# Performance work log

Measured on AMD Instinct MI355X. Metric: run time of the kernel, lower is better.

Reference implementation:

```python
import jax, jax.numpy as jnp
from jax import lax
import numpy as np

GAMMA, WARP = 0.01, 134.4          # SoftDTW(gamma=0.01, warp=134.4)
INF, BIG = 100000.0, 1e9           # INF from kl_loss_sdtw; BIG ~ math.inf boundary
KL_A, KL_FWD_A, GEN_A, GEN_E2E_A, FEAT_A, DUR_A, MEL_A = 1.0, 1.0, 1.0, 1.0, 1.0, 1.0, 45.0


def soft_dtw(D):
    """Soft-DTW with warp penalty. D: [B, N, M] -> R[:, N, M].
    R[i,j] = D[i-1,j-1] + softmin_gamma(R[i-1,j-1], R[i-1,j]+warp, R[i,j-1]+warp)."""
    B, N, M = D.shape
    row0 = jnp.full((B, M + 1), BIG, D.dtype).at[:, 0].set(0.0)  # R[0, :]

    def row_step(prev_row, d_row):                 # prev_row: [B, M+1], d_row: [B, M]
        left0 = jnp.full((B,), BIG, D.dtype)       # R[i, 0]

        def col_step(r_left, inp):
            d, r_diag, r_up = inp                  # each [B]
            r0 = -r_diag / GAMMA
            r1 = -(r_up + WARP) / GAMMA
            r2 = -(r_left + WARP) / GAMMA
            rmax = jnp.maximum(jnp.maximum(r0, r1), r2)
            smin = -GAMMA * (jnp.log(jnp.exp(r0 - rmax) + jnp.exp(r1 - rmax) + jnp.exp(r2 - rmax)) + rmax)
            r = d + smin
            return r, r

        xs = (d_row.T, prev_row[:, :-1].T, prev_row[:, 1:].T)   # scan over j=1..M
        _, vals = lax.scan(col_step, left0, xs)                 # [M, B]
        new_row = jnp.concatenate([left0[:, None], vals.T], axis=1)
        return new_row, None

    last, _ = lax.scan(row_step, row0, jnp.swapaxes(D, 0, 1))   # scan over i=1..N
    return last[:, M]


def sdtw_kl_matrix(z, logs_q, m, logs_p):
    """kl[b,i,j] = sum_h logs_p - logs_q - 0.5 + 0.5*(z-m)^2*exp(-2 logs_p).
    m, logs_p: [b,h,tp]; z, logs_q: [b,h,tq] -> [b,tp,tq] via 3 batched GEMMs."""
    h = m.shape[1]
    w = jnp.exp(-2.0 * logs_p)                                   # [b,h,tp]
    quad = (jnp.einsum('bhi,bhj->bij', w, z * z)
            - 2.0 * jnp.einsum('bhi,bhj->bij', w * m, z)
            + jnp.sum(w * m * m, axis=1)[:, :, None])
    return (jnp.sum(logs_p, axis=1)[:, :, None]
            - jnp.sum(logs_q, axis=1)[:, None, :]
            - 0.5 * h + 0.5 * quad)


def kl_loss_sdtw(z, logs_q, m, logs_p, p_mask, q_mask):
    kl = sdtw_kl_matrix(z, logs_q, m, logs_p)
    kl = jnp.pad(kl, ((0, 0), (0, 1), (0, 1)))
    pm = jnp.pad(p_mask, ((0, 0), (0, 1)))
    qm = jnp.pad(q_mask, ((0, 0), (0, 1)))
    pb = pm[:, :, None].astype(bool)
    qb = qm[:, None, :].astype(bool)
    kl = jnp.where(pb ^ qb, INF, kl)
    kl = jnp.where((~pb) & (~qb), 0.0, kl)
    return jnp.sum(soft_dtw(kl)) / jnp.sum(pm)


def _forward(mel_slice, mel_slice_hat, scores_disc_fake, scores_disc_fake_e2e,
             feats_disc_real, feats_disc_fake, loss_duration, loss_duration_len,
             loss_pitch, z_p, m_p, logs_p, z_q, m_q, logs_q, p_mask, z_mask):
    # generator losses: sum over discriminators of mean((1-score)^2)
    loss_gen = jnp.sum(jnp.mean((1.0 - scores_disc_fake) ** 2, axis=(1, 2))) * GEN_A
    loss_gen_e2e = jnp.sum(jnp.mean((1.0 - scores_disc_fake_e2e) ** 2, axis=(1, 2))) * GEN_E2E_A
    # feature-matching loss (real feats detached)
    fr = lax.stop_gradient(feats_disc_real)
    loss_fm = jnp.sum(jnp.mean(jnp.abs(fr - feats_disc_fake), axis=(1, 2, 3))) * 2.0 * FEAT_A
    loss_mel = jnp.mean(jnp.abs(mel_slice - mel_slice_hat)) * MEL_A
    loss_dur = jnp.sum(loss_duration) * DUR_A
    loss_dur_len = jnp.log(loss_duration_len + 1e-6)
    zm = z_mask[:, 0, :]
    loss_kl = kl_loss_sdtw(z_p, logs_q, m_p, logs_p, p_mask, zm) * KL_A
    loss_kl_fwd = kl_loss_sdtw(z_q, logs_p, m_q, logs_q, zm, p_mask) * KL_FWD_A
    return (loss_gen + loss_gen_e2e + loss_fm + loss_mel + loss_dur
            + loss_dur_len + loss_kl + loss_kl_fwd)


def setup_inputs() -> dict:
    key = jax.random.key(0)
    ks = jax.random.split(key, 16)
    B, H, TP, TQ = 4, 192, 350, 400
    return {
        'mel_slice': jax.random.normal(ks[0], (B, 80, 128), jnp.float32),
        'mel_slice_hat': jax.random.normal(ks[1], (B, 80, 128), jnp.float32),
        'scores_disc_fake': jax.random.normal(ks[2], (6, B, 8192), jnp.float32),
        'scores_disc_fake_e2e': jax.random.normal(ks[3], (6, B, 8192), jnp.float32),
        'feats_disc_real': jax.random.normal(ks[4], (24, B, 128, 4096), jnp.float32),
        'feats_disc_fake': jax.random.normal(ks[5], (24, B, 128, 4096), jnp.float32),
        'loss_duration': jax.random.uniform(ks[6], (B, TP), jnp.float32) * 0.01,
        'loss_duration_len': jax.random.uniform(ks[7], (), jnp.float32) + 0.5,
        'loss_pitch': jax.random.uniform(ks[8], (B, TP), jnp.float32),
        'z_p': jax.random.normal(ks[9], (B, H, TQ), jnp.float32),
        'm_p': jax.random.normal(ks[10], (B, H, TP), jnp.float32),
        'logs_p': 0.1 * jax.random.normal(ks[11], (B, H, TP), jnp.float32),
        'z_q': jax.random.normal(ks[12], (B, H, TP), jnp.float32),
        'm_q': jax.random.normal(ks[13], (B, H, TQ), jnp.float32),
        'logs_q': 0.1 * jax.random.normal(ks[14], (B, H, TQ), jnp.float32),
        'p_mask': jnp.ones((B, TP), jnp.float32),
        'z_mask': jnp.ones((B, 1, TQ), jnp.float32),
    }


def reference(mel_slice, mel_slice_hat, scores_disc_fake, scores_disc_fake_e2e,
              feats_disc_real, feats_disc_fake, loss_duration, loss_duration_len,
              loss_pitch, z_p, m_p, logs_p, z_q, m_q, logs_q, p_mask, z_mask):
    return _forward(mel_slice, mel_slice_hat, scores_disc_fake, scores_disc_fake_e2e,
                    feats_disc_real, feats_disc_fake, loss_duration, loss_duration_len,
                    loss_pitch, z_p, m_p, logs_p, z_q, m_q, logs_q, p_mask, z_mask)
```

## Files before the change

kernel.cpp:

```cpp
#include <hip/hip_runtime.h>
#include <math.h>

#define GAMMA_ 0.01f
#define WARP_  134.4f
#define INFV   100000.0f
#define BIGV   1000000000.0f

#define B_  4
#define H_  192
#define TP_ 350
#define TQ_ 400

#define ACC_OFF 0
#define DTW_OFF 16
#define SLP_OFF 32
#define SLQ_OFF (SLP_OFF + B_*TP_)
#define KL1_OFF 3072
#define KL1_NCOL 401
#define KL1_PITCHT 352
#define KL2_OFF (KL1_OFF + B_*KL1_NCOL*KL1_PITCHT)
#define KL2_NCOL 351
#define KL2_PITCHT 408

#define RING_SLOTS 67
#define RING_PITCH 416

typedef float f4_t __attribute__((ext_vector_type(4)));

__device__ __forceinline__ unsigned pk2(float a, float b) {
    unsigned ua = __float_as_uint(a), ub = __float_as_uint(b);
    ua = (ua + 0x7FFFu + ((ua >> 16) & 1u)) >> 16;
    ub = (ub + 0x7FFFu + ((ub >> 16) & 1u)) & 0xFFFF0000u;
    return ua | ub;
}
__device__ __forceinline__ int modS(int x) { return x - (x / RING_SLOTS) * RING_SLOTS; }

__global__ void sl_kernel(const float* __restrict__ logs_p,
                          const float* __restrict__ logs_q,
                          const float* __restrict__ pmask,
                          const float* __restrict__ zmask,
                          float* __restrict__ ws) {
    if (blockIdx.x == 12) {
        int tid = threadIdx.x;
        float a5 = 0.f, a6 = 0.f;
        for (int v = tid; v < B_ * TP_; v += 256) a5 += pmask[v];
        for (int v = tid; v < B_ * TQ_; v += 256) a6 += zmask[v];
        __shared__ float s5[4], s6[4];
        for (int off = 32; off > 0; off >>= 1) { a5 += __shfl_xor(a5, off); a6 += __shfl_xor(a6, off); }
        if ((tid & 63) == 0) { s5[tid >> 6] = a5; s6[tid >> 6] = a6; }
        __syncthreads();
        if (tid == 0) {
            ws[5] = s5[0] + s5[1] + s5[2] + s5[3];
            ws[6] = s6[0] + s6[1] + s6[2] + s6[3];
        }
        return;
    }
    int t = blockIdx.x * 256 + threadIdx.x;
    if (t < 32 && t != 5 && t != 6) ws[ACC_OFF + t] = 0.f;
    if (t < B_ * TP_) {
        int b = t / TP_, i = t % TP_;
        const float* p = logs_p + (size_t)b * H_ * TP_ + i;
        float s = 0.f;
        for (int h = 0; h < H_; ++h) s += p[(size_t)h * TP_];
        ws[SLP_OFF + t] = s;
    } else if (t < B_ * TP_ + B_ * TQ_) {
        int t2 = t - B_ * TP_;
        int b = t2 / TQ_, j = t2 % TQ_;
        const float* p = logs_q + (size_t)b * H_ * TQ_ + j;
        float s = 0.f;
        for (int h = 0; h < H_; ++h) s += p[(size_t)h * TQ_];
        ws[SLQ_OFF + t2] = s;
    }
}

__global__ void kl_kernel(const float* __restrict__ mp, const float* __restrict__ lsp,
                          const float* __restrict__ zp,
                          const float* __restrict__ mq, const float* __restrict__ lsq,
                          const float* __restrict__ zq,
                          const float* __restrict__ pmask, const float* __restrict__ zmask,
                          float* __restrict__ ws) {
    int which = blockIdx.z >> 2;
    int b     = blockIdx.z & 3;
    const float *mS, *lS, *zS, *SLrow, *SLcol, *rm, *cm; float* out; int R, C, pitchT;
    if (which == 0) { mS=mp; lS=lsp; zS=zp; SLrow=ws+SLP_OFF; SLcol=ws+SLQ_OFF;
                      rm=pmask + b*TP_; cm=zmask + b*TQ_;
                      out=ws+KL1_OFF + (size_t)b*KL1_NCOL*KL1_PITCHT;
                      R=TP_; C=TQ_; pitchT=KL1_PITCHT; }
    else            { mS=mq; lS=lsq; zS=zq; SLrow=ws+SLQ_OFF; SLcol=ws+SLP_OFF;
                      rm=zmask + b*TQ_; cm=pmask + b*TP_;
                      out=ws+KL2_OFF + (size_t)b*KL2_NCOL*KL2_PITCHT;
                      R=TQ_; C=TP_; pitchT=KL2_PITCHT; }
    int i0 = blockIdx.x * 32;
    int j0 = blockIdx.y * 32;
    if (i0 > R || j0 > C) return;
    __shared__ __align__(16) float wS [16][32];
    __shared__ __align__(16) float mSh[16][32];
    __shared__ __align__(16) float zSh[16][32];
    const float* mB = mS + (size_t)b * H_ * R;
    const float* lB = lS + (size_t)b * H_ * R;
    const float* zB = zS + (size_t)b * H_ * C;
    int tx = threadIdx.x, ty = threadIdx.y;
    int t  = ty * 16 + tx;
    float a00 = 0.f, a01 = 0.f, a10 = 0.f, a11 = 0.f;
    for (int h0 = 0; h0 < H_; h0 += 16) {
        for (int e = t; e < 512; e += 256) {
            int hh = e >> 5, cc = e & 31;
            int h = h0 + hh;
            int gi = i0 + cc, gj = j0 + cc;
            float wv = 0.f, mv = 0.f;
            if (gi < R) {
                wv = __expf(-2.f * lB[(size_t)h * R + gi]);
                mv = mB[(size_t)h * R + gi];
            }
            wS[hh][cc] = wv; mSh[hh][cc] = mv;
            zSh[hh][cc] = (gj < C) ? zB[(size_t)h * C + gj] : 0.f;
        }
        __syncthreads();
#pragma unroll
        for (int kk = 0; kk < 16; ++kk) {
            float2 wv = *(const float2*)&wS [kk][tx * 2];
            float2 mv = *(const float2*)&mSh[kk][tx * 2];
            float2 zv = *(const float2*)&zSh[kk][ty * 2];
            float d;
            d = zv.x - mv.x; a00 += wv.x * d * d;
            d = zv.x - mv.y; a01 += wv.y * d * d;
            d = zv.y - mv.x; a10 += wv.x * d * d;
            d = zv.y - mv.y; a11 += wv.y * d * d;
        }
        __syncthreads();
    }
    float accs[2][2] = {{a00, a01}, {a10, a11}};
    for (int jj = 0; jj < 2; ++jj)
        for (int ii = 0; ii < 2; ++ii) {
            int I = i0 + tx * 2 + ii, J = j0 + ty * 2 + jj;
            if (I <= R && J <= C) {
                bool pbI = (I < R) && (rm[I] != 0.f);
                bool qbJ = (J < C) && (cm[J] != 0.f);
                float v;
                if (pbI & qbJ)
                    v = SLrow[b * R + I] - SLcol[b * C + J] - 0.5f * H_ + 0.5f * accs[jj][ii];
                else
                    v = (pbI ^ qbJ) ? INFV : 0.f;
                out[(size_t)J * pitchT + I] = v;
            }
        }
}

#define SLD(q, r, cc, ii, vv) { int col_ = ((q) << 3) + (cc); \
    if ((vv) && col_ <= C_) r = *(const f4_t*)(klT + (size_t)col_ * pitchT + ((ii) << 2)); }
#define SST(q, r, cc, ii, vv) { int col_ = ((q) << 3) + (cc); \
    if ((vv) && col_ <= C_) { int s_ = modS(col_); \
        uint2 u_; u_.x = pk2(r.x, r.y); u_.y = pk2(r.z, r.w); \
        *(uint2*)&ring[s_][(ii) << 2] = u_; } }

__global__ __launch_bounds__(512, 1) void dtw_kernel(float* ws) {
    __shared__ __align__(16) unsigned short ring[RING_SLOTS + 2][RING_PITCH];
    int bid = blockIdx.x, tid = threadIdx.x;
    int b = bid & 3, which = bid >> 2;
    int R_, C_, pitchT;
    const float* klT;
    if (which == 0) {
        R_ = TP_; C_ = TQ_; pitchT = KL1_PITCHT;
        klT = ws + KL1_OFF + (size_t)b * KL1_NCOL * KL1_PITCHT;
    } else {
        R_ = TQ_; C_ = TP_; pitchT = KL2_PITCHT;
        klT = ws + KL2_OFF + (size_t)b * KL2_NCOL * KL2_PITCHT;
    }
    int lres = R_ >> 3;
    int kres = R_ & 7;
    int tmax = C_ + lres;
    int P = (tmax >> 3) + 1;

    if (tid < 64) {
        int lane = tid; bool lane0 = (lane == 0);
        float p0=BIGV,p1=BIGV,p2=BIGV,p3=BIGV,p4=BIGV,p5=BIGV,p6=BIGV,p7=BIGV;
        float recv_cur = BIGV, recv_prev = BIGV;
        __syncthreads();
        for (int ph = 0; ph < P; ++ph) {
            int t0 = ph << 3;
            int c0 = t0 - lane;
            int cr = c0 < 0 ? 0 : (c0 > C_ ? C_ : c0);
            int s0 = modS(cr);
            int4 rd = *(const int4*)&ring[s0][lane << 3];
#pragma unroll
            for (int i = 0; i < 8; ++i) {
                int c = t0 + i - lane;
                int4 ru = rd;
                if (i < 7) {
                    int cn = c + 1; cn = cn < 0 ? 0 : (cn > C_ ? C_ : cn);
                    int sn = modS(cn);
                    rd = *(const int4*)&ring[sn][lane << 3];
                }
                float last_ = 0.f;
                if ((unsigned)c <= (unsigned)C_) {
                    float u_  = lane0 ? BIGV : recv_cur;
                    float dg  = (c == 0) ? (lane0 ? 0.f : BIGV) : (lane0 ? BIGV : recv_prev);
                    float d0 = __uint_as_float((unsigned)ru.x << 16);
                    float d1 = __uint_as_float((unsigned)ru.x & 0xFFFF0000u);
                    float d2 = __uint_as_float((unsigned)ru.y << 16);
                    float d3 = __uint_as_float((unsigned)ru.y & 0xFFFF0000u);
                    float d4 = __uint_as_float((unsigned)ru.z << 16);
                    float d5 = __uint_as_float((unsigned)ru.z & 0xFFFF0000u);
                    float d6 = __uint_as_float((unsigned)ru.w << 16);
                    float d7 = __uint_as_float((unsigned)ru.w & 0xFFFF0000u);
                    float B0 = WARP_ + d0, B1 = WARP_ + d1, B2 = WARP_ + d2, B3 = WARP_ + d3;
                    float B4 = WARP_ + d4, B5 = WARP_ + d5, B6 = WARP_ + d6, B7 = WARP_ + d7;
                    float P0 = fminf(dg + d0, p0 + B0);
                    float P1 = fminf(p0 + d1, p1 + B1);
                    float P2 = fminf(p1 + d2, p2 + B2);
                    float P3 = fminf(p2 + d3, p3 + B3);
                    float P4 = fminf(p3 + d4, p4 + B4);
                    float P5 = fminf(p4 + d5, p5 + B5);
                    float P6 = fminf(p5 + d6, p6 + B6);
                    float P7 = fminf(p6 + d7, p7 + B7);
                    u_ = fminf(P0, u_ + B0); p0 = u_;
                    u_ = fminf(P1, u_ + B1); p1 = u_;
                    u_ = fminf(P2, u_ + B2); p2 = u_;
                    u_ = fminf(P3, u_ + B3); p3 = u_;
                    u_ = fminf(P4, u_ + B4); p4 = u_;
                    u_ = fminf(P5, u_ + B5); p5 = u_;
                    u_ = fminf(P6, u_ + B6); p6 = u_;
                    u_ = fminf(P7, u_ + B7); p7 = u_;
                    last_ = u_;
                }
                recv_prev = recv_cur;
                recv_cur  = __shfl_up(last_, 1);
            }
            __syncthreads();
        }
        float q0 = __shfl(p0, lres), q1 = __shfl(p1, lres), q2 = __shfl(p2, lres),
              q3 = __shfl(p3, lres), q4 = __shfl(p4, lres), q5 = __shfl(p5, lres),
              q6 = __shfl(p6, lres), q7 = __shfl(p7, lres);
        if (lane0) {
            float res = (kres == 0) ? q0 : (kres == 1) ? q1 : (kres == 2) ? q2 :
                        (kres == 3) ? q3 : (kres == 4) ? q4 : (kres == 5) ? q5 :
                        (kres == 6) ? q6 : q7;
            ws[DTW_OFF + which * 4 + b] = res;
        }
    } else {
        int st  = tid - 64;
        int n4  = pitchT >> 2;
        int tot = n4 << 3;
        int cA = st / n4,  iA = st - cA * n4;
        int eB = st + 448; int cB = eB / n4, iB = eB - cB * n4;
        bool vA = st < tot, vB = eB < tot;
        f4_t rA = {0.f,0.f,0.f,0.f}, rB = {0.f,0.f,0.f,0.f};
        SLD(0, rA, cA, iA, vA) SLD(0, rB, cB, iB, vB)
        SST(0, rA, cA, iA, vA) SST(0, rB, cB, iB, vB)
        SLD(1, rA, cA, iA, vA) SLD(1, rB, cB, iB, vB)
        __syncthreads();
        for (int p = 0; p < P; ++p) {
            SST(p + 1, rA, cA, iA, vA) SST(p + 1, rB, cB, iB, vB)
            SLD(p + 2, rA, cA, iA, vA) SLD(p + 2, rB, cB, iB, vB)
            __syncthreads();
        }
    }
}

__global__ __launch_bounds__(512) void red_kernel(
    const float* __restrict__ mel, const float* __restrict__ melh,
    const float* __restrict__ sg,  const float* __restrict__ se,
    const float* __restrict__ fr,  const float* __restrict__ ff,
    const float* __restrict__ dur, float* ws) {
    __shared__ float sb[64];
    int tid = threadIdx.x;
    long T = (long)gridDim.x * 512;
    long gid = (long)blockIdx.x * 512 + tid;
    const float4* fr4   = (const float4*)fr;
    const float4* ff4   = (const float4*)ff;
    const float4* sg4   = (const float4*)sg;
    const float4* se4   = (const float4*)se;
    const float4* mel4  = (const float4*)mel;
    const float4* melh4 = (const float4*)melh;
    const float4* dur4  = (const float4*)dur;
    const long E0 = 12582912;
    float a2 = 0.f;
    long v = gid;
    for (; v + T < E0; v += 2 * T) {
        float4 x0 = fr4[v],     y0 = ff4[v];
        float4 x1 = fr4[v + T], y1 = ff4[v + T];
        a2 += fabsf(x0.x-y0.x)+fabsf(x0.y-y0.y)+fabsf(x0.z-y0.z)+fabsf(x0.w-y0.w);
        a2 += fabsf(x1.x-y1.x)+fabsf(x1.y-y1.y)+fabsf(x1.z-y1.z)+fabsf(x1.w-y1.w);
    }
    for (; v < E0; v += T) {
        float4 x = fr4[v], y = ff4[v];
        a2 += fabsf(x.x-y.x)+fabsf(x.y-y.y)+fabsf(x.z-y.z)+fabsf(x.w-y.w);
    }
    float a0=0.f, a1=0.f, a3=0.f, a4=0.f;
    long w = gid;
    if (w < 108894) {
        if (w < 49152) {
            float4 s = sg4[w]; float e;
            e=1.f-s.x; a0+=e*e; e=1.f-s.y; a0+=e*e; e=1.f-s.z; a0+=e*e; e=1.f-s.w; a0+=e*e;
        } else if (w < 98304) {
            float4 s = se4[w - 49152]; float e;
            e=1.f-s.x; a1+=e*e; e=1.f-s.y; a1+=e*e; e=1.f-s.z; a1+=e*e; e=1.f-s.w; a1+=e*e;
        } else if (w < 108544) {
            float4 x = mel4[w - 98304], y = melh4[w - 98304];
            a3 += fabsf(x.x-y.x)+fabsf(x.y-y.y)+fabsf(x.z-y.z)+fabsf(x.w-y.w);
        } else {
            float4 x = dur4[w - 108544]; a4 += x.x + x.y + x.z + x.w;
        }
    }
    float vals[5] = {a0, a1, a2, a3, a4};
#pragma unroll
    for (int q = 0; q < 5; ++q) {
        float x = vals[q];
        for (int off = 32; off > 0; off >>= 1) x += __shfl_xor(x, off);
        if ((tid & 63) == 0) sb[(tid >> 6) * 8 + q] = x;
    }
    __syncthreads();
    if (tid < 5) {
        float s = 0.f;
        for (int w2 = 0; w2 < 8; ++w2) s += sb[w2 * 8 + tid];
        atomicAdd(&ws[ACC_OFF + tid], s);
    }
}

__global__ void final_kernel(const float* __restrict__ ws,
                             const float* __restrict__ ldl,
                             float* __restrict__ out) {
    if (threadIdx.x == 0 && blockIdx.x == 0) {
        float gen  = ws[0] * (1.f / 32768.f);
        float e2e  = ws[1] * (1.f / 32768.f);
        float fm   = ws[2] * (2.f / 2097152.f);
        float melv = ws[3] * (45.f / 40960.f);
        float durv = ws[4];
        float dlen = logf(ldl[0] + 1e-6f);
        float kl  = (ws[DTW_OFF + 0] + ws[DTW_OFF + 1] + ws[DTW_OFF + 2] + ws[DTW_OFF + 3]) / ws[5];
        float klf = (ws[DTW_OFF + 4] + ws[DTW_OFF + 5] + ws[DTW_OFF + 6] + ws[DTW_OFF + 7]) / ws[6];
        out[0] = gen + e2e + fm + melv + durv + dlen + kl + klf;
    }
}

extern "C" void kernel_launch(void* const* d_in, const int* in_sizes, int n_in,
                              void* d_out, int out_size, void* d_ws, size_t ws_size,
                              hipStream_t stream) {
    const float* mel    = (const float*)d_in[0];
    const float* melh   = (const float*)d_in[1];
    const float* sg     = (const float*)d_in[2];
    const float* se     = (const float*)d_in[3];
    const float* fr     = (const float*)d_in[4];
    const float* ff     = (const float*)d_in[5];
    const float* dur    = (const float*)d_in[6];
    const float* ldl    = (const float*)d_in[7];
    const float* z_p    = (const float*)d_in[9];
    const float* m_p    = (const float*)d_in[10];
    const float* logs_p = (const float*)d_in[11];
    const float* z_q    = (const float*)d_in[12];
    const float* m_q    = (const float*)d_in[13];
    const float* logs_q = (const float*)d_in[14];
    const float* pmask  = (const float*)d_in[15];
    const float* zmask  = (const float*)d_in[16];
    float* ws  = (float*)d_ws;
    float* out = (float*)d_out;

    sl_kernel<<<13, 256, 0, stream>>>(logs_p, logs_q, pmask, zmask, ws);
    kl_kernel<<<dim3(13, 13, 8), dim3(16, 16), 0, stream>>>(
        m_p, logs_p, z_p, m_q, logs_q, z_q, pmask, zmask, ws);
    dtw_kernel<<<8, 512, 0, stream>>>(ws);
    red_kernel<<<1016, 512, 0, stream>>>(mel, melh, sg, se, fr, ff, dur, ws);
    final_kernel<<<1, 64, 0, stream>>>(ws, ldl, out);
}
```

Baseline: 206.6 us.

## Fuse DTW and reduction kernels so serial DTW overlaps bandwidth-bound reduction

Merges the 8-block DTW kernel and the large L1/MSE reduction kernel into one launch. The first 8 blocks run the serial DTW recurrence while the remaining 1016 blocks stream the feature tensors, so the latency-bound DTW hides behind the memory-bound reduction instead of running before it. The reduction also moves to nontemporal loads with a 4-way unroll. Risks: launch_bounds(512,1) now applies to the reduction blocks and may limit their occupancy, and the DTW blocks may share CUs with reduction blocks.

```diff
diff --git a/kernel.cpp b/kernel.cpp
--- a/kernel.cpp
+++ b/kernel.cpp
@@ -153,167 +153,176 @@
         uint2 u_; u_.x = pk2(r.x, r.y); u_.y = pk2(r.z, r.w); \
         *(uint2*)&ring[s_][(ii) << 2] = u_; } }
 
-__global__ __launch_bounds__(512, 1) void dtw_kernel(float* ws) {
-    __shared__ __align__(16) unsigned short ring[RING_SLOTS + 2][RING_PITCH];
-    int bid = blockIdx.x, tid = threadIdx.x;
-    int b = bid & 3, which = bid >> 2;
-    int R_, C_, pitchT;
-    const float* klT;
-    if (which == 0) {
-        R_ = TP_; C_ = TQ_; pitchT = KL1_PITCHT;
-        klT = ws + KL1_OFF + (size_t)b * KL1_NCOL * KL1_PITCHT;
-    } else {
-        R_ = TQ_; C_ = TP_; pitchT = KL2_PITCHT;
-        klT = ws + KL2_OFF + (size_t)b * KL2_NCOL * KL2_PITCHT;
-    }
-    int lres = R_ >> 3;
-    int kres = R_ & 7;
-    int tmax = C_ + lres;
-    int P = (tmax >> 3) + 1;
-
-    if (tid < 64) {
-        int lane = tid; bool lane0 = (lane == 0);
-        float p0=BIGV,p1=BIGV,p2=BIGV,p3=BIGV,p4=BIGV,p5=BIGV,p6=BIGV,p7=BIGV;
-        float recv_cur = BIGV, recv_prev = BIGV;
-        __syncthreads();
-        for (int ph = 0; ph < P; ++ph) {
-            int t0 = ph << 3;
-            int c0 = t0 - lane;
-            int cr = c0 < 0 ? 0 : (c0 > C_ ? C_ : c0);
-            int s0 = modS(cr);
-            int4 rd = *(const int4*)&ring[s0][lane << 3];
-#pragma unroll
-            for (int i = 0; i < 8; ++i) {
-                int c = t0 + i - lane;
-                int4 ru = rd;
-                if (i < 7) {
-                    int cn = c + 1; cn = cn < 0 ? 0 : (cn > C_ ? C_ : cn);
-                    int sn = modS(cn);
-                    rd = *(const int4*)&ring[sn][lane << 3];
-                }
-                float last_ = 0.f;
-                if ((unsigned)c <= (unsigned)C_) {
-                    float u_  = lane0 ? BIGV : recv_cur;
-                    float dg  = (c == 0) ? (lane0 ? 0.f : BIGV) : (lane0 ? BIGV : recv_prev);
-                    float d0 = __uint_as_float((unsigned)ru.x << 16);
-                    float d1 = __uint_as_float((unsigned)ru.x & 0xFFFF0000u);
-                    float d2 = __uint_as_float((unsigned)ru.y << 16);
-                    float d3 = __uint_as_float((unsigned)ru.y & 0xFFFF0000u);
-                    float d4 = __uint_as_float((unsigned)ru.z << 16);
-                    float d5 = __uint_as_float((unsigned)ru.z & 0xFFFF0000u);
-                    float d6 = __uint_as_float((unsigned)ru.w << 16);
-                    float d7 = __uint_as_float((unsigned)ru.w & 0xFFFF0000u);
-                    float B0 = WARP_ + d0, B1 = WARP_ + d1, B2 = WARP_ + d2, B3 = WARP_ + d3;
-                    float B4 = WARP_ + d4, B5 = WARP_ + d5, B6 = WARP_ + d6, B7 = WARP_ + d7;
-                    float P0 = fminf(dg + d0, p0 + B0);
-                    float P1 = fminf(p0 + d1, p1 + B1);
-                    float P2 = fminf(p1 + d2, p2 + B2);
-                    float P3 = fminf(p2 + d3, p3 + B3);
-                    float P4 = fminf(p3 + d4, p4 + B4);
-                    float P5 = fminf(p4 + d5, p5 + B5);
-                    float P6 = fminf(p5 + d6, p6 + B6);
-                    float P7 = fminf(p6 + d7, p7 + B7);
-                    u_ = fminf(P0, u_ + B0); p0 = u_;
-                    u_ = fminf(P1, u_ + B1); p1 = u_;
-                    u_ = fminf(P2, u_ + B2); p2 = u_;
-                    u_ = fminf(P3, u_ + B3); p3 = u_;
-                    u_ = fminf(P4, u_ + B4); p4 = u_;
-                    u_ = fminf(P5, u_ + B5); p5 = u_;
-                    u_ = fminf(P6, u_ + B6); p6 = u_;
-                    u_ = fminf(P7, u_ + B7); p7 = u_;
-                    last_ = u_;
-                }
-                recv_prev = recv_cur;
-                recv_cur  = __shfl_up(last_, 1);
-            }
-            __syncthreads();
-        }
-        float q0 = __shfl(p0, lres), q1 = __shfl(p1, lres), q2 = __shfl(p2, lres),
-              q3 = __shfl(p3, lres), q4 = __shfl(p4, lres), q5 = __shfl(p5, lres),
-              q6 = __shfl(p6, lres), q7 = __shfl(p7, lres);
-        if (lane0) {
-            float res = (kres == 0) ? q0 : (kres == 1) ? q1 : (kres == 2) ? q2 :
-                        (kres == 3) ? q3 : (kres == 4) ? q4 : (kres == 5) ? q5 :
-                        (kres == 6) ? q6 : q7;
-            ws[DTW_OFF + which * 4 + b] = res;
-        }
-    } else {
-        int st  = tid - 64;
-        int n4  = pitchT >> 2;
-        int tot = n4 << 3;
-        int cA = st / n4,  iA = st - cA * n4;
-        int eB = st + 448; int cB = eB / n4, iB = eB - cB * n4;
-        bool vA = st < tot, vB = eB < tot;
-        f4_t rA = {0.f,0.f,0.f,0.f}, rB = {0.f,0.f,0.f,0.f};
-        SLD(0, rA, cA, iA, vA) SLD(0, rB, cB, iB, vB)
-        SST(0, rA, cA, iA, vA) SST(0, rB, cB, iB, vB)
-        SLD(1, rA, cA, iA, vA) SLD(1, rB, cB, iB, vB)
-        __syncthreads();
-        for (int p = 0; p < P; ++p) {
-            SST(p + 1, rA, cA, iA, vA) SST(p + 1, rB, cB, iB, vB)
-            SLD(p + 2, rA, cA, iA, vA) SLD(p + 2, rB, cB, iB, vB)
-            __syncthreads();
-        }
-    }
-}
-
-__global__ __launch_bounds__(512) void red_kernel(
+__global__ __launch_bounds__(512, 1) void main_kernel(
     const float* __restrict__ mel, const float* __restrict__ melh,
     const float* __restrict__ sg,  const float* __restrict__ se,
     const float* __restrict__ fr,  const float* __restrict__ ff,
     const float* __restrict__ dur, float* ws) {
-    __shared__ float sb[64];
-    int tid = threadIdx.x;
-    long T = (long)gridDim.x * 512;
-    long gid = (long)blockIdx.x * 512 + tid;
-    const float4* fr4   = (const float4*)fr;
-    const float4* ff4   = (const float4*)ff;
-    const float4* sg4   = (const float4*)sg;
-    const float4* se4   = (const float4*)se;
-    const float4* mel4  = (const float4*)mel;
-    const float4* melh4 = (const float4*)melh;
-    const float4* dur4  = (const float4*)dur;
-    const long E0 = 12582912;
-    float a2 = 0.f;
-    long v = gid;
-    for (; v + T < E0; v += 2 * T) {
-        float4 x0 = fr4[v],     y0 = ff4[v];
-        float4 x1 = fr4[v + T], y1 = ff4[v + T];
-        a2 += fabsf(x0.x-y0.x)+fabsf(x0.y-y0.y)+fabsf(x0.z-y0.z)+fabsf(x0.w-y0.w);
-        a2 += fabsf(x1.x-y1.x)+fabsf(x1.y-y1.y)+fabsf(x1.z-y1.z)+fabsf(x1.w-y1.w);
-    }
-    for (; v < E0; v += T) {
-        float4 x = fr4[v], y = ff4[v];
-        a2 += fabsf(x.x-y.x)+fabsf(x.y-y.y)+fabsf(x.z-y.z)+fabsf(x.w-y.w);
-    }
-    float a0=0.f, a1=0.f, a3=0.f, a4=0.f;
-    long w = gid;
-    if (w < 108894) {
-        if (w < 49152) {
-            float4 s = sg4[w]; float e;
-            e=1.f-s.x; a0+=e*e; e=1.f-s.y; a0+=e*e; e=1.f-s.z; a0+=e*e; e=1.f-s.w; a0+=e*e;
-        } else if (w < 98304) {
-            float4 s = se4[w - 49152]; float e;
-            e=1.f-s.x; a1+=e*e; e=1.f-s.y; a1+=e*e; e=1.f-s.z; a1+=e*e; e=1.f-s.w; a1+=e*e;
-        } else if (w < 108544) {
-            float4 x = mel4[w - 98304], y = melh4[w - 98304];
-            a3 += fabsf(x.x-y.x)+fabsf(x.y-y.y)+fabsf(x.z-y.z)+fabsf(x.w-y.w);
+    __shared__ __align__(16) unsigned short ring[RING_SLOTS + 2][RING_PITCH];
+    int bid = blockIdx.x, tid = threadIdx.x;
+    if (bid < 8) {
+        int b = bid & 3, which = bid >> 2;
+        int R_, C_, pitchT;
+        const float* klT;
+        if (which == 0) {
+            R_ = TP_; C_ = TQ_; pitchT = KL1_PITCHT;
+            klT = ws + KL1_OFF + (size_t)b * KL1_NCOL * KL1_PITCHT;
         } else {
-            float4 x = dur4[w - 108544]; a4 += x.x + x.y + x.z + x.w;
-        }
-    }
-    float vals[5] = {a0, a1, a2, a3, a4};
+            R_ = TQ_; C_ = TP_; pitchT = KL2_PITCHT;
+            klT = ws + KL2_OFF + (size_t)b * KL2_NCOL * KL2_PITCHT;
+        }
+        int lres = R_ >> 3;
+        int kres = R_ & 7;
+        int tmax = C_ + lres;
+        int P = (tmax >> 3) + 1;
+
+        if (tid < 64) {
+            int lane = tid; bool lane0 = (lane == 0);
+            float p0=BIGV,p1=BIGV,p2=BIGV,p3=BIGV,p4=BIGV,p5=BIGV,p6=BIGV,p7=BIGV;
+            float recv_cur = BIGV, recv_prev = BIGV;
+            __syncthreads();
+            for (int ph = 0; ph < P; ++ph) {
+                int t0 = ph << 3;
+                int c0 = t0 - lane;
+                int cr = c0 < 0 ? 0 : (c0 > C_ ? C_ : c0);
+                int s0 = modS(cr);
+                int4 rd = *(const int4*)&ring[s0][lane << 3];
 #pragma unroll
-    for (int q = 0; q < 5; ++q) {
-        float x = vals[q];
-        for (int off = 32; off > 0; off >>= 1) x += __shfl_xor(x, off);
-        if ((tid & 63) == 0) sb[(tid >> 6) * 8 + q] = x;
-    }
-    __syncthreads();
-    if (tid < 5) {
-        float s = 0.f;
-        for (int w2 = 0; w2 < 8; ++w2) s += sb[w2 * 8 + tid];
-        atomicAdd(&ws[ACC_OFF + tid], s);
+                for (int i = 0; i < 8; ++i) {
+                    int c = t0 + i - lane;
+                    int4 ru = rd;
+                    if (i < 7) {
+                        int cn = c + 1; cn = cn < 0 ? 0 : (cn > C_ ? C_ : cn);
+                        int sn = modS(cn);
+                        rd = *(const int4*)&ring[sn][lane << 3];
+                    }
+                    float last_ = 0.f;
+                    if ((unsigned)c <= (unsigned)C_) {
+                        float u_  = lane0 ? BIGV : recv_cur;
+                        float dg  = (c == 0) ? (lane0 ? 0.f : BIGV) : (lane0 ? BIGV : recv_prev);
+                        float d0 = __uint_as_float((unsigned)ru.x << 16);
+                        float d1 = __uint_as_float((unsigned)ru.x & 0xFFFF0000u);
+                        float d2 = __uint_as_float((unsigned)ru.y << 16);
+                        float d3 = __uint_as_float((unsigned)ru.y & 0xFFFF0000u);
+                        float d4 = __uint_as_float((unsigned)ru.z << 16);
+                        float d5 = __uint_as_float((unsigned)ru.z & 0xFFFF0000u);
+                        float d6 = __uint_as_float((unsigned)ru.w << 16);
+                        float d7 = __uint_as_float((unsigned)ru.w & 0xFFFF0000u);
+                        float B0 = WARP_ + d0, B1 = WARP_ + d1, B2 = WARP_ + d2, B3 = WARP_ + d3;
+                        float B4 = WARP_ + d4, B5 = WARP_ + d5, B6 = WARP_ + d6, B7 = WARP_ + d7;
+                        float P0 = fminf(dg + d0, p0 + B0);
+                        float P1 = fminf(p0 + d1, p1 + B1);
+                        float P2 = fminf(p1 + d2, p2 + B2);
+                        float P3 = fminf(p2 + d3, p3 + B3);
+                        float P4 = fminf(p3 + d4, p4 + B4);
+                        float P5 = fminf(p4 + d5, p5 + B5);
+                        float P6 = fminf(p5 + d6, p6 + B6);
+                        float P7 = fminf(p6 + d7, p7 + B7);
+                        u_ = fminf(P0, u_ + B0); p0 = u_;
+                        u_ = fminf(P1, u_ + B1); p1 = u_;
+                        u_ = fminf(P2, u_ + B2); p2 = u_;
+                        u_ = fminf(P3, u_ + B3); p3 = u_;
+                        u_ = fminf(P4, u_ + B4); p4 = u_;
+                        u_ = fminf(P5, u_ + B5); p5 = u_;
+                        u_ = fminf(P6, u_ + B6); p6 = u_;
+                        u_ = fminf(P7, u_ + B7); p7 = u_;
+                        last_ = u_;
+                    }
+                    recv_prev = recv_cur;
+                    recv_cur  = __shfl_up(last_, 1);
+                }
+                __syncthreads();
+            }
+            float q0 = __shfl(p0, lres), q1 = __shfl(p1, lres), q2 = __shfl(p2, lres),
+                  q3 = __shfl(p3, lres), q4 = __shfl(p4, lres), q5 = __shfl(p5, lres),
+                  q6 = __shfl(p6, lres), q7 = __shfl(p7, lres);
+            if (lane0) {
+                float res = (kres == 0) ? q0 : (kres == 1) ? q1 : (kres == 2) ? q2 :
+                            (kres == 3) ? q3 : (kres == 4) ? q4 : (kres == 5) ? q5 :
+                            (kres == 6) ? q6 : q7;
+                ws[DTW_OFF + which * 4 + b] = res;
+            }
+        } else {
+            int st  = tid - 64;
+            int n4  = pitchT >> 2;
+            int tot = n4 << 3;
+            int cA = st / n4,  iA = st - cA * n4;
+            int eB = st + 448; int cB = eB / n4, iB = eB - cB * n4;
+            bool vA = st < tot, vB = eB < tot;
+            f4_t rA = {0.f,0.f,0.f,0.f}, rB = {0.f,0.f,0.f,0.f};
+            SLD(0, rA, cA, iA, vA) SLD(0, rB, cB, iB, vB)
+            SST(0, rA, cA, iA, vA) SST(0, rB, cB, iB, vB)
+            SLD(1, rA, cA, iA, vA) SLD(1, rB, cB, iB, vB)
+            __syncthreads();
+            for (int p = 0; p < P; ++p) {
+                SST(p + 1, rA, cA, iA, vA) SST(p + 1, rB, cB, iB, vB)
+                SLD(p + 2, rA, cA, iA, vA) SLD(p + 2, rB, cB, iB, vB)
+                __syncthreads();
+            }
+        }
+    } else {
+        int rid = bid - 8;
+        long T = (long)(gridDim.x - 8) * 512;
+        long gid = (long)rid * 512 + tid;
+        const f4_t* fr4   = (const f4_t*)fr;
+        const f4_t* ff4   = (const f4_t*)ff;
+        const float4* sg4   = (const float4*)sg;
+        const float4* se4   = (const float4*)se;
+        const float4* mel4  = (const float4*)mel;
+        const float4* melh4 = (const float4*)melh;
+        const float4* dur4  = (const float4*)dur;
+        const long E0 = 12582912;
+        float a2 = 0.f;
+        long v = gid;
+        for (; v + 3 * T < E0; v += 4 * T) {
+            f4_t x0 = __builtin_nontemporal_load(fr4 + v);
+            f4_t y0 = __builtin_nontemporal_load(ff4 + v);
+            f4_t x1 = __builtin_nontemporal_load(fr4 + v + T);
+            f4_t y1 = __builtin_nontemporal_load(ff4 + v + T);
+            f4_t x2 = __builtin_nontemporal_load(fr4 + v + 2 * T);
+            f4_t y2 = __builtin_nontemporal_load(ff4 + v + 2 * T);
+            f4_t x3 = __builtin_nontemporal_load(fr4 + v + 3 * T);
+            f4_t y3 = __builtin_nontemporal_load(ff4 + v + 3 * T);
+            a2 += fabsf(x0.x-y0.x)+fabsf(x0.y-y0.y)+fabsf(x0.z-y0.z)+fabsf(x0.w-y0.w);
+            a2 += fabsf(x1.x-y1.x)+fabsf(x1.y-y1.y)+fabsf(x1.z-y1.z)+fabsf(x1.w-y1.w);
+            a2 += fabsf(x2.x-y2.x)+fabsf(x2.y-y2.y)+fabsf(x2.z-y2.z)+fabsf(x2.w-y2.w);
+            a2 += fabsf(x3.x-y3.x)+fabsf(x3.y-y3.y)+fabsf(x3.z-y3.z)+fabsf(x3.w-y3.w);
+        }
+        for (; v < E0; v += T) {
+            f4_t x = __builtin_nontemporal_load(fr4 + v);
+            f4_t y = __builtin_nontemporal_load(ff4 + v);
+            a2 += fabsf(x.x-y.x)+fabsf(x.y-y.y)+fabsf(x.z-y.z)+fabsf(x.w-y.w);
+        }
+        float a0=0.f, a1=0.f, a3=0.f, a4=0.f;
+        long w = gid;
+        if (w < 108894) {
+            if (w < 49152) {
+                float4 s = sg4[w]; float e;
+                e=1.f-s.x; a0+=e*e; e=1.f-s.y; a0+=e*e; e=1.f-s.z; a0+=e*e; e=1.f-s.w; a0+=e*e;
+            } else if (w < 98304) {
+                float4 s = se4[w - 49152]; float e;
+                e=1.f-s.x; a1+=e*e; e=1.f-s.y; a1+=e*e; e=1.f-s.z; a1+=e*e; e=1.f-s.w; a1+=e*e;
+            } else if (w < 108544) {
+                float4 x = mel4[w - 98304], y = melh4[w - 98304];
+                a3 += fabsf(x.x-y.x)+fabsf(x.y-y.y)+fabsf(x.z-y.z)+fabsf(x.w-y.w);
+            } else {
+                float4 x = dur4[w - 108544]; a4 += x.x + x.y + x.z + x.w;
+            }
+        }
+        float vals[5] = {a0, a1, a2, a3, a4};
+        float* sb = (float*)ring;
+#pragma unroll
+        for (int q = 0; q < 5; ++q) {
+            float x = vals[q];
+            for (int off = 32; off > 0; off >>= 1) x += __shfl_xor(x, off);
+            if ((tid & 63) == 0) sb[(tid >> 6) * 8 + q] = x;
+        }
+        __syncthreads();
+        if (tid < 5) {
+            float s = 0.f;
+            for (int w2 = 0; w2 < 8; ++w2) s += sb[w2 * 8 + tid];
+            atomicAdd(&ws[ACC_OFF + tid], s);
+        }
     }
 }
 
@@ -358,7 +367,6 @@
     sl_kernel<<<13, 256, 0, stream>>>(logs_p, logs_q, pmask, zmask, ws);
     kl_kernel<<<dim3(13, 13, 8), dim3(16, 16), 0, stream>>>(
         m_p, logs_p, z_p, m_q, logs_q, z_q, pmask, zmask, ws);
-    dtw_kernel<<<8, 512, 0, stream>>>(ws);
-    red_kernel<<<1016, 512, 0, stream>>>(mel, melh, sg, se, fr, ff, dur, ws);
+    main_kernel<<<8 + 1016, 512, 0, stream>>>(mel, melh, sg, se, fr, ff, dur, ws);
     final_kernel<<<1, 64, 0, stream>>>(ws, ldl, out);
 }
```

Measured after the change: 169.0 us. 18.2% less time.
